# Kernel optimization log

Hardware: AMD Instinct MI355X
Metric: run time of the kernel (lower is better)

Reference implementation:

```python
import jax, jax.numpy as jnp
import numpy as np
import math

EPS = 1e-4

def _l2_normalize(a, eps=EPS):
    # torch F.normalize: a / max(||a||_2, eps)
    n = jnp.linalg.norm(a, axis=-1, keepdims=True)
    return a / jnp.maximum(n, eps)

def setup_inputs() -> dict:
    key = jax.random.key(0)
    k1, k2 = jax.random.split(key)
    N, D, K = 32768, 256, 32
    x = jax.random.normal(k1, (N, D), dtype=jnp.float32)
    mu = jax.random.normal(k2, (K, D), dtype=jnp.float32)
    kappa = jnp.full((K,), 10.0, dtype=jnp.float32)
    return {"x": x, "mu": mu, "kappa": kappa}

def reference(x, mu, kappa):
    N, D = x.shape
    K = mu.shape[0]
    x_norm = _l2_normalize(x)              # (N, D)
    mu_norm = _l2_normalize(mu)            # (K, D)
    kappa_pos = jnp.clip(kappa, EPS, None) # (K,)
    c = x_norm @ mu_norm.T                 # (N, K) cosine similarities
    gamma = jax.nn.softmax(kappa_pos[None, :] * c, axis=-1)  # (N, K)
    # tangent (first-order) gradient, broadcast to (N, K, D)
    v = x_norm[:, None, :] - c[:, :, None] * mu_norm[None, :, :]
    denom = jnp.sqrt(1.0 - c[:, :, None] ** 2 + EPS)
    G_mu = gamma[:, :, None] * jnp.sqrt(kappa_pos)[None, :, None] * (v / denom)
    G_mu_flat = G_mu.reshape(N, K * D)
    # concentration (second-order) gradient (N, K)
    inv_sqrt2 = 1.0 / math.sqrt(2.0)
    G_kappa = gamma * inv_sqrt2 * (kappa_pos[None, :] * (1.0 - c) - 1.0)
    phi_patches = jnp.concatenate([G_mu_flat, G_kappa], axis=-1)  # (N, K*D+K)
    phi = phi_patches.mean(axis=0)                                 # (K*D+K,)
    return phi
```

## Files before the change

kernel.cpp:

```cpp
#include <hip/hip_runtime.h>

#define EPSF 1e-4f

typedef __attribute__((ext_vector_type(8))) short short8;
typedef __attribute__((ext_vector_type(4))) float f32x4;

#define PSTR 4160u

#define LDS_TOTAL 47616

static __device__ __forceinline__ unsigned short f2bf(float f) {
    unsigned u = __float_as_uint(f);
    u += 0x7fffu + ((u >> 16) & 1u);
    return (unsigned short)(u >> 16);
}
static __device__ __forceinline__ float bflo(unsigned v) { return __uint_as_float(v << 16); }
static __device__ __forceinline__ float bfhi(unsigned v) { return __uint_as_float(v & 0xffff0000u); }

__global__ void __launch_bounds__(256, 2)
spf_main(const float* __restrict__ x, const float* __restrict__ mu,
         const float* __restrict__ kappa, unsigned* __restrict__ P, int ntiles) {
    __shared__ char lds[LDS_TOTAL];
    unsigned short* mun = (unsigned short*)lds;
    f32x4* cbase = (f32x4*)(lds + 16896);
    const int tid = threadIdx.x;
    const int wid = tid >> 6, lane = tid & 63;
    const int l15 = lane & 15, g = lane >> 4;
    unsigned short* wTw = (unsigned short*)(lds + 37376 + wid * 2560);
    const int dbase = wid * 64;

    {
        float* red = (float*)(lds + 16896);
        float* invl = red + 256;
        const int kk = tid >> 3, part = tid & 7;
        const float4* row = (const float4*)(mu + kk * 256 + part * 32);
        float4 v[8];
        float s = 0.f;
        #pragma unroll
        for (int j = 0; j < 8; ++j) {
            v[j] = row[j];
            s += v[j].x * v[j].x + v[j].y * v[j].y + v[j].z * v[j].z + v[j].w * v[j].w;
        }
        red[tid] = s;
        __syncthreads();
        if (tid < 32) {
            float tot = 0.f;
            #pragma unroll
            for (int j = 0; j < 8; ++j) tot += red[tid * 8 + j];
            invl[tid] = 1.0f / fmaxf(sqrtf(tot), EPSF);
        }
        __syncthreads();
        const float inv = invl[kk];
        #pragma unroll
        for (int j = 0; j < 8; ++j) {
            ushort4 b = { f2bf(v[j].x * inv), f2bf(v[j].y * inv),
                          f2bf(v[j].z * inv), f2bf(v[j].w * inv) };
            *(ushort4*)(mun + kk * 264 + part * 32 + j * 4) = b;
        }
    }
    const float kp0 = fmaxf(kappa[l15], EPSF);
    const float kp1 = fmaxf(kappa[16 + l15], EPSF);
    __syncthreads();

    const f32x4 fz = {0.f, 0.f, 0.f, 0.f};
    f32x4 acc[2][4];
    #pragma unroll
    for (int h = 0; h < 2; ++h)
        #pragma unroll
        for (int dt = 0; dt < 4; ++dt)
            acc[h][dt] = fz;
    float S0 = 0.f, S1 = 0.f, G0 = 0.f, G1 = 0.f;

    for (int tile = blockIdx.x; tile < ntiles; tile += gridDim.x) {
        const float* xt = x + (size_t)tile * (32 * 256);

        f32x4 cc00 = fz, cc01 = fz, cc10 = fz, cc11 = fz;
        float ss0 = 0.f, ss1 = 0.f;
        #pragma unroll
        for (int ch = 0; ch < 2; ++ch) {
            const int off = dbase + ch * 32 + g * 8;
            float4 p0 = *(const float4*)(xt + l15 * 256 + off);
            float4 p1 = *(const float4*)(xt + l15 * 256 + off + 4);
            float4 q0 = *(const float4*)(xt + (16 + l15) * 256 + off);
            float4 q1 = *(const float4*)(xt + (16 + l15) * 256 + off + 4);
            ss0 += p0.x*p0.x + p0.y*p0.y + p0.z*p0.z + p0.w*p0.w
                 + p1.x*p1.x + p1.y*p1.y + p1.z*p1.z + p1.w*p1.w;
            ss1 += q0.x*q0.x + q0.y*q0.y + q0.z*q0.z + q0.w*q0.w
                 + q1.x*q1.x + q1.y*q1.y + q1.z*q1.z + q1.w*q1.w;
            short8 a0, a1;
            a0[0]=(short)f2bf(p0.x); a0[1]=(short)f2bf(p0.y); a0[2]=(short)f2bf(p0.z); a0[3]=(short)f2bf(p0.w);
            a0[4]=(short)f2bf(p1.x); a0[5]=(short)f2bf(p1.y); a0[6]=(short)f2bf(p1.z); a0[7]=(short)f2bf(p1.w);
            a1[0]=(short)f2bf(q0.x); a1[1]=(short)f2bf(q0.y); a1[2]=(short)f2bf(q0.z); a1[3]=(short)f2bf(q0.w);
            a1[4]=(short)f2bf(q1.x); a1[5]=(short)f2bf(q1.y); a1[6]=(short)f2bf(q1.z); a1[7]=(short)f2bf(q1.w);
            short8 b0 = *(const short8*)(mun + l15 * 264 + off);
            short8 b1 = *(const short8*)(mun + (16 + l15) * 264 + off);
            cc00 = __builtin_amdgcn_mfma_f32_16x16x32_bf16(a0, b0, cc00, 0, 0, 0);
            cc01 = __builtin_amdgcn_mfma_f32_16x16x32_bf16(a0, b1, cc01, 0, 0, 0);
            cc10 = __builtin_amdgcn_mfma_f32_16x16x32_bf16(a1, b0, cc10, 0, 0, 0);
            cc11 = __builtin_amdgcn_mfma_f32_16x16x32_bf16(a1, b1, cc11, 0, 0, 0);
        }

        float xf[4][8];
        #pragma unroll
        for (int dt = 0; dt < 4; ++dt)
            #pragma unroll
            for (int e = 0; e < 8; ++e)
                xf[dt][e] = xt[(g * 8 + e) * 256 + dbase + dt * 16 + l15];
        short8 xb[4];
        #pragma unroll
        for (int dt = 0; dt < 4; ++dt)
            #pragma unroll
            for (int e = 0; e < 8; ++e)
                xb[dt][e] = (short)f2bf(xf[dt][e]);

        {
            f32x4* cw = cbase + (wid * 5) * 64 + lane;
            cw[0] = cc00; cw[64] = cc01; cw[128] = cc10; cw[192] = cc11;
            *(float2*)(cw + 256) = make_float2(ss0, ss1);
        }
        __syncthreads();
        f32x4 C00 = fz, C01 = fz, C10 = fz, C11 = fz;
        float SS0 = 0.f, SS1 = 0.f;
        #pragma unroll
        for (int w2 = 0; w2 < 4; ++w2) {
            const f32x4* cr = cbase + (w2 * 5) * 64 + lane;
            C00 += cr[0]; C01 += cr[64]; C10 += cr[128]; C11 += cr[192];
            float2 sv = *(const float2*)(cr + 256);
            SS0 += sv.x; SS1 += sv.y;
        }
        __syncthreads();
        SS0 += __shfl_xor(SS0, 16); SS0 += __shfl_xor(SS0, 32);
        SS1 += __shfl_xor(SS1, 16); SS1 += __shfl_xor(SS1, 32);
        const float inv0 = 1.0f / fmaxf(sqrtf(SS0), EPSF);
        const float inv1 = 1.0f / fmaxf(sqrtf(SS1), EPSF);

        #pragma unroll
        for (int sub = 0; sub < 2; ++sub) {
            const f32x4 ck0 = sub ? C10 : C00;
            const f32x4 ck1 = sub ? C11 : C01;
            const float invsel = sub ? inv1 : inv0;
            #pragma unroll
            for (int r = 0; r < 4; ++r) {
                const float invr = __shfl(invsel, 4 * g + r);
                const float c0 = ck0[r] * invr;
                const float c1 = ck1[r] * invr;
                const float l0 = kp0 * c0, l1 = kp1 * c1;
                float m = fmaxf(l0, l1);
                m = fmaxf(m, __shfl_xor(m, 1));
                m = fmaxf(m, __shfl_xor(m, 2));
                m = fmaxf(m, __shfl_xor(m, 4));
                m = fmaxf(m, __shfl_xor(m, 8));
                const float e0 = __expf(l0 - m), e1 = __expf(l1 - m);
                float z = e0 + e1;
                z += __shfl_xor(z, 1);
                z += __shfl_xor(z, 2);
                z += __shfl_xor(z, 4);
                z += __shfl_xor(z, 8);
                const float rz = 1.0f / z;
                const float g0 = e0 * rz, g1 = e1 * rz;
                const float u0 = g0 * rsqrtf(fmaxf(1.0f - c0 * c0 + EPSF, 1e-12f));
                const float u1 = g1 * rsqrtf(fmaxf(1.0f - c1 * c1 + EPSF, 1e-12f));
                S0 += u0 * c0; S1 += u1 * c1;
                G0 += g0 * (kp0 * (1.0f - c0) - 1.0f);
                G1 += g1 * (kp1 * (1.0f - c1) - 1.0f);
                const int srow = sub * 16 + 4 * g + r;
                wTw[l15 * 40 + srow]        = f2bf(u0 * invr);
                wTw[(16 + l15) * 40 + srow] = f2bf(u1 * invr);
            }
        }

        const short8 wa0 = *(const short8*)(wTw + l15 * 40 + g * 8);
        const short8 wa1 = *(const short8*)(wTw + (16 + l15) * 40 + g * 8);
        #pragma unroll
        for (int dt = 0; dt < 4; ++dt) {
            acc[0][dt] = __builtin_amdgcn_mfma_f32_16x16x32_bf16(wa0, xb[dt], acc[0][dt], 0, 0, 0);
            acc[1][dt] = __builtin_amdgcn_mfma_f32_16x16x32_bf16(wa1, xb[dt], acc[1][dt], 0, 0, 0);
        }
    }

    S0 += __shfl_xor(S0, 16); S0 += __shfl_xor(S0, 32);
    S1 += __shfl_xor(S1, 16); S1 += __shfl_xor(S1, 32);
    G0 += __shfl_xor(G0, 16); G0 += __shfl_xor(G0, 32);
    G1 += __shfl_xor(G1, 16); G1 += __shfl_xor(G1, 32);
    unsigned* Pb = P + (size_t)blockIdx.x * PSTR;
    #pragma unroll
    for (int dt = 0; dt < 4; ++dt)
        #pragma unroll
        for (int r = 0; r < 4; ++r) {
            unsigned lo = f2bf(acc[0][dt][r]);
            unsigned hi = f2bf(acc[1][dt][r]);
            Pb[(4 * g + r) * 256 + dbase + dt * 16 + l15] = (hi << 16) | lo;
        }
    if (wid == 0 && lane < 16) {
        float* Sf = (float*)(Pb + 4096);
        Sf[lane] = S0; Sf[16 + lane] = S1;
        Sf[32 + lane] = G0; Sf[48 + lane] = G1;
    }
}

__global__ void __launch_bounds__(256)
spf_fin(const unsigned* __restrict__ P, const float* __restrict__ mu,
        const float* __restrict__ kappa, float* __restrict__ out, int nb, float invN) {
    __shared__ float r0[256], r1[256];
    const int b = blockIdx.x, t = threadIdx.x;
    if (b < 256) {
        const int kp = b >> 4, dc = b & 15;
        const int dd = t & 15, bq = t >> 4;
        const int d = dc * 16 + dd;
        float A0 = 0.f, A1 = 0.f;
        for (int b2 = bq; b2 < nb; b2 += 16) {
            unsigned v = P[(size_t)b2 * PSTR + kp * 256 + d];
            A0 += bflo(v); A1 += bfhi(v);
        }
        r0[t] = A0; r1[t] = A1;
        __syncthreads();
        #pragma unroll
        for (int off = 128; off >= 16; off >>= 1) {
            if (t < off) { r0[t] += r0[t + off]; r1[t] += r1[t + off]; }
            __syncthreads();
        }
        const float A0f = r0[dd], A1f = r1[dd];
        __syncthreads();
        float s0 = 0.f, s1 = 0.f;
        for (int b2 = t; b2 < nb; b2 += 256) {
            const float* Sf = (const float*)(P + (size_t)b2 * PSTR + 4096);
            s0 += Sf[kp]; s1 += Sf[16 + kp];
        }
        r0[t] = s0; r1[t] = s1;
        __syncthreads();
        #pragma unroll
        for (int off = 128; off >= 1; off >>= 1) {
            if (t < off) { r0[t] += r0[t + off]; r1[t] += r1[t + off]; }
            __syncthreads();
        }
        const float Sk0 = r0[0], Sk1 = r1[0];
        __syncthreads();
        const float m0 = mu[kp * 256 + t], m1 = mu[(16 + kp) * 256 + t];
        r0[t] = m0 * m0; r1[t] = m1 * m1;
        __syncthreads();
        #pragma unroll
        for (int off = 128; off >= 1; off >>= 1) {
            if (t < off) { r0[t] += r0[t + off]; r1[t] += r1[t + off]; }
            __syncthreads();
        }
        const float inv0 = 1.0f / fmaxf(sqrtf(r0[0]), EPSF);
        const float inv1 = 1.0f / fmaxf(sqrtf(r1[0]), EPSF);
        if (t < 16) {
            const float sq0 = sqrtf(fmaxf(kappa[kp], EPSF));
            const float sq1 = sqrtf(fmaxf(kappa[16 + kp], EPSF));
            const int dO = dc * 16 + t;
            out[kp * 256 + dO]        = sq0 * (A0f - Sk0 * mu[kp * 256 + dO] * inv0) * invN;
            out[(16 + kp) * 256 + dO] = sq1 * (A1f - Sk1 * mu[(16 + kp) * 256 + dO] * inv1) * invN;
        }
    } else {
        const int k = t & 31, bq = t >> 5;
        float gs = 0.f;
        for (int b2 = bq; b2 < nb; b2 += 8) {
            const float* Gf = (const float*)(P + (size_t)b2 * PSTR + 4096);
            gs += Gf[32 + k];
        }
        r0[t] = gs;
        __syncthreads();
        #pragma unroll
        for (int off = 128; off >= 32; off >>= 1) {
            if (t < off) r0[t] += r0[t + off];
            __syncthreads();
        }
        if (t < 32) out[8192 + t] = r0[t] * 0.70710678118654752f * invN;
    }
}

extern "C" void kernel_launch(void* const* d_in, const int* in_sizes, int n_in,
                              void* d_out, int out_size, void* d_ws, size_t ws_size,
                              hipStream_t stream) {
    const float* x = (const float*)d_in[0];
    const float* mu = (const float*)d_in[1];
    const float* kappa = (const float*)d_in[2];
    unsigned* P = (unsigned*)d_ws;
    float* out = (float*)d_out;
    const int N = in_sizes[0] / 256;
    const int ntiles = N / 32;
    int nb = ntiles < 512 ? ntiles : 512;
    while (nb > 1 && (size_t)nb * PSTR * 4 > ws_size) nb >>= 1;

    spf_main<<<nb, 256, 0, stream>>>(x, mu, kappa, P, ntiles);
    spf_fin<<<257, 256, 0, stream>>>(P, mu, kappa, out, nb, 1.0f / (float)N);
}
```

Baseline: 40.59 us.

## Use 512-thread blocks with contiguous tile ranges and register prefetch of next tile

New measurement: 37.76 us. -7.0%, faster.

```diff
diff --git a/kernel.cpp b/kernel.cpp
--- a/kernel.cpp
+++ b/kernel.cpp
@@ -7,7 +7,7 @@
 
 #define PSTR 4160u
 
-#define LDS_TOTAL 47616
+#define LDS_TOTAL 78336
 
 static __device__ __forceinline__ unsigned short f2bf(float f) {
     unsigned u = __float_as_uint(f);
@@ -17,7 +17,7 @@
 static __device__ __forceinline__ float bflo(unsigned v) { return __uint_as_float(v << 16); }
 static __device__ __forceinline__ float bfhi(unsigned v) { return __uint_as_float(v & 0xffff0000u); }
 
-__global__ void __launch_bounds__(256, 2)
+__global__ void __launch_bounds__(512, 2)
 spf_main(const float* __restrict__ x, const float* __restrict__ mu,
          const float* __restrict__ kappa, unsigned* __restrict__ P, int ntiles) {
     __shared__ char lds[LDS_TOTAL];
@@ -26,18 +26,18 @@
     const int tid = threadIdx.x;
     const int wid = tid >> 6, lane = tid & 63;
     const int l15 = lane & 15, g = lane >> 4;
-    unsigned short* wTw = (unsigned short*)(lds + 37376 + wid * 2560);
-    const int dbase = wid * 64;
+    unsigned short* wTw = (unsigned short*)(lds + 57856 + wid * 2560);
+    const int dbase = wid * 32;
 
     {
         float* red = (float*)(lds + 16896);
-        float* invl = red + 256;
-        const int kk = tid >> 3, part = tid & 7;
-        const float4* row = (const float4*)(mu + kk * 256 + part * 32);
-        float4 v[8];
+        float* invl = red + 512;
+        const int kk = tid >> 4, part = tid & 15;
+        const float4* row = (const float4*)(mu + kk * 256 + part * 16);
+        float4 v[4];
         float s = 0.f;
         #pragma unroll
-        for (int j = 0; j < 8; ++j) {
+        for (int j = 0; j < 4; ++j) {
             v[j] = row[j];
             s += v[j].x * v[j].x + v[j].y * v[j].y + v[j].z * v[j].z + v[j].w * v[j].w;
         }
@@ -46,16 +46,16 @@
         if (tid < 32) {
             float tot = 0.f;
             #pragma unroll
-            for (int j = 0; j < 8; ++j) tot += red[tid * 8 + j];
+            for (int j = 0; j < 16; ++j) tot += red[tid * 16 + j];
             invl[tid] = 1.0f / fmaxf(sqrtf(tot), EPSF);
         }
         __syncthreads();
         const float inv = invl[kk];
         #pragma unroll
-        for (int j = 0; j < 8; ++j) {
+        for (int j = 0; j < 4; ++j) {
             ushort4 b = { f2bf(v[j].x * inv), f2bf(v[j].y * inv),
                           f2bf(v[j].z * inv), f2bf(v[j].w * inv) };
-            *(ushort4*)(mun + kk * 264 + part * 32 + j * 4) = b;
+            *(ushort4*)(mun + kk * 264 + part * 16 + j * 4) = b;
         }
     }
     const float kp0 = fmaxf(kappa[l15], EPSF);
@@ -63,55 +63,54 @@
     __syncthreads();
 
     const f32x4 fz = {0.f, 0.f, 0.f, 0.f};
-    f32x4 acc[2][4];
-    #pragma unroll
-    for (int h = 0; h < 2; ++h)
-        #pragma unroll
-        for (int dt = 0; dt < 4; ++dt)
-            acc[h][dt] = fz;
+    f32x4 acc00 = fz, acc01 = fz, acc10 = fz, acc11 = fz;
     float S0 = 0.f, S1 = 0.f, G0 = 0.f, G1 = 0.f;
 
-    for (int tile = blockIdx.x; tile < ntiles; tile += gridDim.x) {
-        const float* xt = x + (size_t)tile * (32 * 256);
-
-        f32x4 cc00 = fz, cc01 = fz, cc10 = fz, cc11 = fz;
-        float ss0 = 0.f, ss1 = 0.f;
-        #pragma unroll
-        for (int ch = 0; ch < 2; ++ch) {
-            const int off = dbase + ch * 32 + g * 8;
-            float4 p0 = *(const float4*)(xt + l15 * 256 + off);
-            float4 p1 = *(const float4*)(xt + l15 * 256 + off + 4);
-            float4 q0 = *(const float4*)(xt + (16 + l15) * 256 + off);
-            float4 q1 = *(const float4*)(xt + (16 + l15) * 256 + off + 4);
-            ss0 += p0.x*p0.x + p0.y*p0.y + p0.z*p0.z + p0.w*p0.w
-                 + p1.x*p1.x + p1.y*p1.y + p1.z*p1.z + p1.w*p1.w;
-            ss1 += q0.x*q0.x + q0.y*q0.y + q0.z*q0.z + q0.w*q0.w
-                 + q1.x*q1.x + q1.y*q1.y + q1.z*q1.z + q1.w*q1.w;
-            short8 a0, a1;
-            a0[0]=(short)f2bf(p0.x); a0[1]=(short)f2bf(p0.y); a0[2]=(short)f2bf(p0.z); a0[3]=(short)f2bf(p0.w);
-            a0[4]=(short)f2bf(p1.x); a0[5]=(short)f2bf(p1.y); a0[6]=(short)f2bf(p1.z); a0[7]=(short)f2bf(p1.w);
-            a1[0]=(short)f2bf(q0.x); a1[1]=(short)f2bf(q0.y); a1[2]=(short)f2bf(q0.z); a1[3]=(short)f2bf(q0.w);
-            a1[4]=(short)f2bf(q1.x); a1[5]=(short)f2bf(q1.y); a1[6]=(short)f2bf(q1.z); a1[7]=(short)f2bf(q1.w);
-            short8 b0 = *(const short8*)(mun + l15 * 264 + off);
-            short8 b1 = *(const short8*)(mun + (16 + l15) * 264 + off);
-            cc00 = __builtin_amdgcn_mfma_f32_16x16x32_bf16(a0, b0, cc00, 0, 0, 0);
-            cc01 = __builtin_amdgcn_mfma_f32_16x16x32_bf16(a0, b1, cc01, 0, 0, 0);
-            cc10 = __builtin_amdgcn_mfma_f32_16x16x32_bf16(a1, b0, cc10, 0, 0, 0);
-            cc11 = __builtin_amdgcn_mfma_f32_16x16x32_bf16(a1, b1, cc11, 0, 0, 0);
-        }
-
-        float xf[4][8];
-        #pragma unroll
-        for (int dt = 0; dt < 4; ++dt)
-            #pragma unroll
-            for (int e = 0; e < 8; ++e)
-                xf[dt][e] = xt[(g * 8 + e) * 256 + dbase + dt * 16 + l15];
-        short8 xb[4];
-        #pragma unroll
-        for (int dt = 0; dt < 4; ++dt)
-            #pragma unroll
-            for (int e = 0; e < 8; ++e)
-                xb[dt][e] = (short)f2bf(xf[dt][e]);
+    const int nbk = gridDim.x;
+    const int tpb = ntiles / nbk, rem = ntiles % nbk;
+    const int t0 = blockIdx.x * tpb + (blockIdx.x < rem ? blockIdx.x : rem);
+    const int cnt = tpb + (blockIdx.x < rem ? 1 : 0);
+
+    const int rowA = l15 * 256 + dbase + g * 8;
+    const int rowB = rowA + 16 * 256;
+    const float* xt = x + (size_t)t0 * 8192;
+    float4 p0, p1, q0, q1;
+    if (cnt > 0) {
+        p0 = *(const float4*)(xt + rowA); p1 = *(const float4*)(xt + rowA + 4);
+        q0 = *(const float4*)(xt + rowB); q1 = *(const float4*)(xt + rowB + 4);
+    }
+
+    for (int it = 0; it < cnt; ++it) {
+        const float* xcur = xt;
+        const float4 cp0 = p0, cp1 = p1, cq0 = q0, cq1 = q1;
+        xt += 8192;
+        if (it + 1 < cnt) {
+            p0 = *(const float4*)(xt + rowA); p1 = *(const float4*)(xt + rowA + 4);
+            q0 = *(const float4*)(xt + rowB); q1 = *(const float4*)(xt + rowB + 4);
+        }
+
+        float ss0 = cp0.x*cp0.x + cp0.y*cp0.y + cp0.z*cp0.z + cp0.w*cp0.w
+                  + cp1.x*cp1.x + cp1.y*cp1.y + cp1.z*cp1.z + cp1.w*cp1.w;
+        float ss1 = cq0.x*cq0.x + cq0.y*cq0.y + cq0.z*cq0.z + cq0.w*cq0.w
+                  + cq1.x*cq1.x + cq1.y*cq1.y + cq1.z*cq1.z + cq1.w*cq1.w;
+        short8 a0, a1;
+        a0[0]=(short)f2bf(cp0.x); a0[1]=(short)f2bf(cp0.y); a0[2]=(short)f2bf(cp0.z); a0[3]=(short)f2bf(cp0.w);
+        a0[4]=(short)f2bf(cp1.x); a0[5]=(short)f2bf(cp1.y); a0[6]=(short)f2bf(cp1.z); a0[7]=(short)f2bf(cp1.w);
+        a1[0]=(short)f2bf(cq0.x); a1[1]=(short)f2bf(cq0.y); a1[2]=(short)f2bf(cq0.z); a1[3]=(short)f2bf(cq0.w);
+        a1[4]=(short)f2bf(cq1.x); a1[5]=(short)f2bf(cq1.y); a1[6]=(short)f2bf(cq1.z); a1[7]=(short)f2bf(cq1.w);
+        const short8 b0 = *(const short8*)(mun + l15 * 264 + dbase + g * 8);
+        const short8 b1 = *(const short8*)(mun + (16 + l15) * 264 + dbase + g * 8);
+        f32x4 cc00 = __builtin_amdgcn_mfma_f32_16x16x32_bf16(a0, b0, fz, 0, 0, 0);
+        f32x4 cc01 = __builtin_amdgcn_mfma_f32_16x16x32_bf16(a0, b1, fz, 0, 0, 0);
+        f32x4 cc10 = __builtin_amdgcn_mfma_f32_16x16x32_bf16(a1, b0, fz, 0, 0, 0);
+        f32x4 cc11 = __builtin_amdgcn_mfma_f32_16x16x32_bf16(a1, b1, fz, 0, 0, 0);
+
+        float xf0[8], xf1[8];
+        #pragma unroll
+        for (int e = 0; e < 8; ++e) {
+            xf0[e] = xcur[(g * 8 + e) * 256 + dbase + l15];
+            xf1[e] = xcur[(g * 8 + e) * 256 + dbase + 16 + l15];
+        }
 
         {
             f32x4* cw = cbase + (wid * 5) * 64 + lane;
@@ -122,7 +121,7 @@
         f32x4 C00 = fz, C01 = fz, C10 = fz, C11 = fz;
         float SS0 = 0.f, SS1 = 0.f;
         #pragma unroll
-        for (int w2 = 0; w2 < 4; ++w2) {
+        for (int w2 = 0; w2 < 8; ++w2) {
             const f32x4* cr = cbase + (w2 * 5) * 64 + lane;
             C00 += cr[0]; C01 += cr[64]; C10 += cr[128]; C11 += cr[192];
             float2 sv = *(const float2*)(cr + 256);
@@ -133,6 +132,13 @@
         SS1 += __shfl_xor(SS1, 16); SS1 += __shfl_xor(SS1, 32);
         const float inv0 = 1.0f / fmaxf(sqrtf(SS0), EPSF);
         const float inv1 = 1.0f / fmaxf(sqrtf(SS1), EPSF);
+
+        short8 xb0, xb1;
+        #pragma unroll
+        for (int e = 0; e < 8; ++e) {
+            xb0[e] = (short)f2bf(xf0[e]);
+            xb1[e] = (short)f2bf(xf1[e]);
+        }
 
         #pragma unroll
         for (int sub = 0; sub < 2; ++sub) {
@@ -171,11 +177,10 @@
 
         const short8 wa0 = *(const short8*)(wTw + l15 * 40 + g * 8);
         const short8 wa1 = *(const short8*)(wTw + (16 + l15) * 40 + g * 8);
-        #pragma unroll
-        for (int dt = 0; dt < 4; ++dt) {
-            acc[0][dt] = __builtin_amdgcn_mfma_f32_16x16x32_bf16(wa0, xb[dt], acc[0][dt], 0, 0, 0);
-            acc[1][dt] = __builtin_amdgcn_mfma_f32_16x16x32_bf16(wa1, xb[dt], acc[1][dt], 0, 0, 0);
-        }
+        acc00 = __builtin_amdgcn_mfma_f32_16x16x32_bf16(wa0, xb0, acc00, 0, 0, 0);
+        acc01 = __builtin_amdgcn_mfma_f32_16x16x32_bf16(wa0, xb1, acc01, 0, 0, 0);
+        acc10 = __builtin_amdgcn_mfma_f32_16x16x32_bf16(wa1, xb0, acc10, 0, 0, 0);
+        acc11 = __builtin_amdgcn_mfma_f32_16x16x32_bf16(wa1, xb1, acc11, 0, 0, 0);
     }
 
     S0 += __shfl_xor(S0, 16); S0 += __shfl_xor(S0, 32);
@@ -184,13 +189,12 @@
     G1 += __shfl_xor(G1, 16); G1 += __shfl_xor(G1, 32);
     unsigned* Pb = P + (size_t)blockIdx.x * PSTR;
     #pragma unroll
-    for (int dt = 0; dt < 4; ++dt)
-        #pragma unroll
-        for (int r = 0; r < 4; ++r) {
-            unsigned lo = f2bf(acc[0][dt][r]);
-            unsigned hi = f2bf(acc[1][dt][r]);
-            Pb[(4 * g + r) * 256 + dbase + dt * 16 + l15] = (hi << 16) | lo;
-        }
+    for (int r = 0; r < 4; ++r) {
+        unsigned lo0 = f2bf(acc00[r]), hi0 = f2bf(acc10[r]);
+        unsigned lo1 = f2bf(acc01[r]), hi1 = f2bf(acc11[r]);
+        Pb[(4 * g + r) * 256 + dbase + l15]      = (hi0 << 16) | lo0;
+        Pb[(4 * g + r) * 256 + dbase + 16 + l15] = (hi1 << 16) | lo1;
+    }
     if (wid == 0 && lane < 16) {
         float* Sf = (float*)(Pb + 4096);
         Sf[lane] = S0; Sf[16 + lane] = S1;
@@ -280,9 +284,9 @@
     float* out = (float*)d_out;
     const int N = in_sizes[0] / 256;
     const int ntiles = N / 32;
-    int nb = ntiles < 512 ? ntiles : 512;
+    int nb = ntiles < 256 ? ntiles : 256;
     while (nb > 1 && (size_t)nb * PSTR * 4 > ws_size) nb >>= 1;
 
-    spf_main<<<nb, 256, 0, stream>>>(x, mu, kappa, P, ntiles);
+    spf_main<<<nb, 512, 0, stream>>>(x, mu, kappa, P, ntiles);
     spf_fin<<<257, 256, 0, stream>>>(P, mu, kappa, out, nb, 1.0f / (float)N);
 }
```
